# Kernel optimization log

Measured on AMD Instinct MI355X. Metric: run time of the kernel, lower is better.

## Reference

```python
import jax, jax.numpy as jnp
import numpy as np

B, S, D, H = 2, 2048, 1024, 16
DK = D // H


def setup_inputs() -> dict:
    key = jax.random.key(0)
    ks = jax.random.split(key, 11)
    s = 1.0 / np.sqrt(D)
    inp = {
        "q": jax.random.normal(ks[0], (B, S, D), jnp.float32),
        "k": jax.random.normal(ks[1], (B, S, D), jnp.float32),
        "v": jax.random.normal(ks[2], (B, S, D), jnp.float32),
        "mask": jnp.tril(jnp.ones((S, S), jnp.int32))[None, None],  # [1,1,S,S] causal
        "Wq": jax.random.normal(ks[3], (D, D), jnp.float32) * s,
        "bq": jnp.zeros((D,), jnp.float32),
        "Wk": jax.random.normal(ks[4], (D, D), jnp.float32) * s,
        "bk": jnp.zeros((D,), jnp.float32),
        "Wv": jax.random.normal(ks[5], (D, D), jnp.float32) * s,
        "bv": jnp.zeros((D,), jnp.float32),
        "Wo": jax.random.normal(ks[6], (D, D), jnp.float32) * s,
        "bo": jnp.zeros((D,), jnp.float32),
    }
    return inp


def reference(q, k, v, mask, Wq, bq, Wk, bk, Wv, bv, Wo, bo):
    # projections -> [B, H, S, DK]
    def split_heads(x):
        return x.reshape(B, S, H, DK).transpose(0, 2, 1, 3)

    Q = split_heads(q @ Wq + bq)
    K = split_heads(k @ Wk + bk)
    V = split_heads(v @ Wv + bv)

    scores = jnp.einsum("bhqd,bhkd->bhqk", Q, K) / jnp.sqrt(jnp.float32(DK))
    scores = jnp.where(mask == 0, jnp.float32(-1e9), scores)
    # source applies dropout(p=0.0) here -> identity
    attn = jax.nn.softmax(scores, axis=-1)  # [B,H,S,S]
    x = jnp.einsum("bhqk,bhkd->bhqd", attn, V)
    x = x.transpose(0, 2, 1, 3).reshape(B, S, D)
    return x @ Wo + bo
```

## Files before the change

kernel.cpp:

```cpp
#include <hip/hip_runtime.h>
#include <hip/hip_bf16.h>
#include <stdint.h>

#define Bb 2
#define Ss 2048
#define Dd 1024
#define Hh 16
#define DKk 64

#define QSCALE 0.180336878f

typedef __attribute__((ext_vector_type(8))) short s8v;
typedef __attribute__((ext_vector_type(4))) short s4v;
typedef __attribute__((ext_vector_type(4))) float f4v;
typedef __attribute__((ext_vector_type(16))) float f16v;

#if __has_builtin(__builtin_amdgcn_exp2f)
#define EXP2(x) __builtin_amdgcn_exp2f(x)
#else
#define EXP2(x) __expf((x)*0.69314718f)
#endif

__device__ __forceinline__ unsigned short f2bf(float f) {
    __hip_bfloat16 h = __float2bfloat16(f);
    union { __hip_bfloat16 h; unsigned short u; } c; c.h = h;
    return c.u;
}

__device__ __forceinline__ unsigned pack_bf2(float lo, float hi) {
    __hip_bfloat162 h = __float22bfloat162_rn(float2{lo, hi});
    union { __hip_bfloat162 h; unsigned u; } c; c.h = h;
    return c.u;
}

__device__ __forceinline__ void gload16(const void* g, void* l) {
    __builtin_amdgcn_global_load_lds((__attribute__((address_space(1))) void*)g,
                                     (__attribute__((address_space(3))) void*)l, 16, 0, 0);
}

__global__ void __launch_bounds__(256) prep_x(const float* __restrict__ q,
                                              const float* __restrict__ k,
                                              const float* __restrict__ v,
                                              unsigned short* __restrict__ xq,
                                              unsigned short* __restrict__ xk,
                                              unsigned short* __restrict__ xv) {
    const int z = blockIdx.z;
    const float* s = (z == 0) ? q : ((z == 1) ? k : v);
    unsigned short* d = (z == 0) ? xq : ((z == 1) ? xk : xv);
    long i = ((long)blockIdx.x * blockDim.x + threadIdx.x) * 8;
    f4v a = *(const f4v*)(s + i);
    f4v b = *(const f4v*)(s + i + 4);
    union { unsigned u[4]; s8v v; } o;
    o.u[0] = pack_bf2(a[0], a[1]);
    o.u[1] = pack_bf2(a[2], a[3]);
    o.u[2] = pack_bf2(b[0], b[1]);
    o.u[3] = pack_bf2(b[2], b[3]);
    *(s8v*)(void*)(d + i) = o.v;
}

__global__ void __launch_bounds__(256) prep_w(const float* __restrict__ Wq,
                                              const float* __restrict__ Wk,
                                              const float* __restrict__ Wv,
                                              const float* __restrict__ Wo,
                                              unsigned short* __restrict__ o0,
                                              unsigned short* __restrict__ o1,
                                              unsigned short* __restrict__ o2,
                                              unsigned short* __restrict__ o3) {
    __shared__ float t[64][65];
    const int z = blockIdx.z;
    const float* W = (z == 0) ? Wq : ((z == 1) ? Wk : ((z == 2) ? Wv : Wo));
    unsigned short* O = (z == 0) ? o0 : ((z == 1) ? o1 : ((z == 2) ? o2 : o3));
    const int n0 = (blockIdx.x & 15) * 64;
    const int k0 = (blockIdx.x >> 4) * 64;
    const int c = threadIdx.x & 63;
    const int r4 = threadIdx.x >> 6;
#pragma unroll
    for (int i = 0; i < 16; i++) {
        int r = i * 4 + r4;
        t[r][c] = W[(long)(k0 + r) * Dd + n0 + c];
    }
    __syncthreads();
#pragma unroll
    for (int i = 0; i < 16; i++) {
        int r = i * 4 + r4;
        O[(long)(n0 + r) * Dd + k0 + c] = f2bf(t[c][r]);
    }
}

template <int MODE>
__device__ __forceinline__ void gemm_body(const unsigned short* __restrict__ A,
                                          const unsigned short* __restrict__ Bt,
                                          const float* __restrict__ bias,
                                          void* __restrict__ out, float oscale,
                                          unsigned short* smem) {
    unsigned short* As = smem;
    unsigned short* Bs = smem + 128 * 64;
    const int tid = threadIdx.x;
    const int l = tid & 63;
    const int w = tid >> 6;
    const int wr = w >> 1, wc = w & 1;
    const int lr = l & 15, lg = l >> 4;
    const int m0 = blockIdx.y * 128;
    const int n0 = blockIdx.x * 128;

    f4v acc[4][4];
#pragma unroll
    for (int m = 0; m < 4; m++)
#pragma unroll
        for (int n = 0; n < 4; n++) acc[m][n] = (f4v){0.f, 0.f, 0.f, 0.f};

    const int srow = tid >> 3;
    const int sg = (tid & 7) ^ (srow & 7);
    char* lbaseA = (char*)As + w * 1024;
    char* lbaseB = (char*)Bs + w * 1024;

    for (int t = 0; t < 16; t++) {
        const int k0 = t * 64;
#pragma unroll
        for (int i = 0; i < 4; i++) {
            int rowA = i * 32 + srow;
            gload16((const char*)A + ((long)(m0 + rowA) * 1024 + k0) * 2 + sg * 16,
                    lbaseA + i * 4096);
            gload16((const char*)Bt + ((long)(n0 + rowA) * 1024 + k0) * 2 + sg * 16,
                    lbaseB + i * 4096);
        }
        __syncthreads();
#pragma unroll
        for (int kk = 0; kk < 2; kk++) {
            s8v af[4], bfr[4];
#pragma unroll
            for (int m = 0; m < 4; m++) {
                int row = wr * 64 + m * 16 + lr;
                int gc = (kk * 4 + lg) ^ (row & 7);
                af[m] = *(const s8v*)((const char*)As + row * 128 + gc * 16);
            }
#pragma unroll
            for (int n = 0; n < 4; n++) {
                int row = wc * 64 + n * 16 + lr;
                int gc = (kk * 4 + lg) ^ (row & 7);
                bfr[n] = *(const s8v*)((const char*)Bs + row * 128 + gc * 16);
            }
#pragma unroll
            for (int m = 0; m < 4; m++)
#pragma unroll
                for (int n = 0; n < 4; n++)
                    acc[m][n] = __builtin_amdgcn_mfma_f32_16x16x32_bf16(af[m], bfr[n],
                                                                        acc[m][n], 0, 0, 0);
        }
        __syncthreads();
    }

#pragma unroll
    for (int n = 0; n < 4; n++) {
        int col = n0 + wc * 64 + n * 16 + lr;
        float bv = bias[col];
#pragma unroll
        for (int m = 0; m < 4; m++) {
#pragma unroll
            for (int r = 0; r < 4; r++) {
                int row = m0 + wr * 64 + m * 16 + lg * 4 + r;
                float val = acc[m][n][r] + bv;
                if (MODE == 0) {
                    int b = row >> 11, s2 = row & 2047, h = col >> 6, d = col & 63;
                    ((unsigned short*)out)[(((b * Hh + h) * Ss + s2) << 6) + d] =
                        f2bf(val * oscale);
                } else if (MODE == 1) {
                    int b = row >> 11, s2 = row & 2047, h = col >> 6, d = col & 63;
                    ((unsigned short*)out)[((b * Hh + h) * DKk + d) * Ss + s2] = f2bf(val);
                } else {
                    ((float*)out)[(long)row * Dd + col] = val;
                }
            }
        }
    }
}

__global__ void __launch_bounds__(256) qkv_gemm(const unsigned short* __restrict__ xq,
                                                const unsigned short* __restrict__ xk,
                                                const unsigned short* __restrict__ xv,
                                                const unsigned short* __restrict__ Wqt,
                                                const unsigned short* __restrict__ Wkt,
                                                const unsigned short* __restrict__ Wvt,
                                                const float* __restrict__ bq,
                                                const float* __restrict__ bk,
                                                const float* __restrict__ bv,
                                                unsigned short* __restrict__ Qh,
                                                unsigned short* __restrict__ Kh,
                                                unsigned short* __restrict__ Vt) {
    __shared__ unsigned short smem[128 * 64 * 2];
    const int z = blockIdx.z;
    if (z == 0)
        gemm_body<0>(xq, Wqt, bq, Qh, QSCALE, smem);
    else if (z == 1)
        gemm_body<0>(xk, Wkt, bk, Kh, 1.f, smem);
    else
        gemm_body<1>(xv, Wvt, bv, Vt, 1.f, smem);
}

__global__ void __launch_bounds__(256) out_gemm(const unsigned short* __restrict__ x,
                                                const unsigned short* __restrict__ Wot,
                                                const float* __restrict__ bo,
                                                float* __restrict__ out) {
    __shared__ unsigned short smem[128 * 64 * 2];
    gemm_body<2>(x, Wot, bo, out, 1.f, smem);
}

__global__ void __launch_bounds__(256) attn_kernel(const unsigned short* __restrict__ Qh,
                                                   const unsigned short* __restrict__ Kh,
                                                   const unsigned short* __restrict__ Vt,
                                                   unsigned short* __restrict__ xatt) {
    __shared__ __align__(16) char ldsbuf[32768];
    unsigned short* Ks = (unsigned short*)ldsbuf;
    unsigned short* Vs = (unsigned short*)(ldsbuf + 16384);
    const int tid = threadIdx.x;
    const int w = tid >> 6, l = tid & 63;
    const int lq = l & 31;
    const int hi = l >> 5;
    const int bh = blockIdx.x & 31;
    const int tile = 63 - (blockIdx.x >> 5);
    const int q0 = tile * 32;
    const int b = bh >> 4, h = bh & 15;
    const unsigned short* Qp = Qh + bh * Ss * DKk;
    const unsigned short* Kp = Kh + bh * Ss * DKk;
    const unsigned short* Vp = Vt + bh * DKk * Ss;

    s8v qf[4];
#pragma unroll
    for (int kk = 0; kk < 4; kk++)
        qf[kk] = *(const s8v*)(Qp + (q0 + lq) * 64 + kk * 16 + hi * 8);

    f16v oT0, oT1;
#pragma unroll
    for (int r = 0; r < 16; r++) { oT0[r] = 0.f; oT1[r] = 0.f; }
    float mx = -1e30f, sm = 0.f;
    const int nkb = tile + 1;
    const int nch = (nkb + 3) >> 2;

    for (int ch = 0; ch < nch; ch++) {
        const int kv0 = ch * 128;
#pragma unroll
        for (int i = 0; i < 4; i++) {
            const int G0 = i * 256 + w * 64;
            int G = G0 + l;
            int row = G >> 3, gd = G & 7;
            int gs = gd ^ (row & 7);
            gload16(Kp + (kv0 + row) * 64 + gs * 8, (char*)Ks + G0 * 16);
        }
#pragma unroll
        for (int i = 0; i < 4; i++) {
            const int G0 = i * 256 + w * 64;
            int G = G0 + l;
            int row = G >> 4, gd = G & 15;
            int gs = gd ^ (row & 15);
            gload16(Vp + (long)row * Ss + kv0 + gs * 8, (char*)Vs + G0 * 16);
        }
        __syncthreads();

        const int kb = ch * 4 + w;
        if (kb < nkb) {
            const int k0 = kb * 32;
            s8v kf[4];
#pragma unroll
            for (int kk = 0; kk < 4; kk++) {
                int row = w * 32 + lq;
                int g = (2 * kk + hi) ^ (row & 7);
                kf[kk] = *(const s8v*)((const char*)Ks + (row * 8 + g) * 16);
            }
            s8v vf0[2], vf1[2];
#pragma unroll
            for (int kk = 0; kk < 2; kk++) {
                int g0 = 4 * w + 2 * kk + hi;
                vf0[kk] = *(const s8v*)((const char*)Vs + (lq * 16 + (g0 ^ (lq & 15))) * 16);
                vf1[kk] =
                    *(const s8v*)((const char*)Vs + ((32 + lq) * 16 + (g0 ^ (lq & 15))) * 16);
            }

            f16v S;
#pragma unroll
            for (int r = 0; r < 16; r++) S[r] = 0.f;
#pragma unroll
            for (int kk = 0; kk < 4; kk++)
                S = __builtin_amdgcn_mfma_f32_32x32x16_bf16(kf[kk], qf[kk], S, 0, 0, 0);

            const bool diag = (kb == nkb - 1);
            float e[16];
#pragma unroll
            for (int r = 0; r < 16; r++) {
                float v = S[r];
                if (diag) {
                    int kv = k0 + (r & 3) + 8 * (r >> 2) + 4 * hi;
                    if (kv > q0 + lq) v = -1e30f;
                }
                e[r] = v;
            }
            float m8[8];
#pragma unroll
            for (int i = 0; i < 8; i++) m8[i] = fmaxf(e[i], e[i + 8]);
#pragma unroll
            for (int i = 0; i < 4; i++) m8[i] = fmaxf(m8[i], m8[i + 4]);
            float pmax = fmaxf(fmaxf(m8[0], m8[1]), fmaxf(m8[2], m8[3]));
            pmax = fmaxf(pmax, __shfl_xor(pmax, 32));

            if (!__all(pmax - mx <= 8.f)) {
                float mn = fmaxf(mx, pmax);
                float sc = EXP2(mx - mn);
                mx = mn;
                sm *= sc;
#pragma unroll
                for (int r = 0; r < 16; r++) { oT0[r] *= sc; oT1[r] *= sc; }
            }
#pragma unroll
            for (int r = 0; r < 16; r++) e[r] = EXP2(e[r] - mx);
            float s8s[8];
#pragma unroll
            for (int i = 0; i < 8; i++) s8s[i] = e[i] + e[i + 8];
#pragma unroll
            for (int i = 0; i < 4; i++) s8s[i] = s8s[i] + s8s[i + 4];
            float rs = (s8s[0] + s8s[1]) + (s8s[2] + s8s[3]);
            sm += rs + __shfl_xor(rs, 32);

            unsigned pk[8], sw[8];
#pragma unroll
            for (int i = 0; i < 8; i++) pk[i] = pack_bf2(e[2 * i], e[2 * i + 1]);
#pragma unroll
            for (int i = 0; i < 8; i++) sw[i] = (unsigned)__shfl_xor((int)pk[i], 32);
            union { unsigned u[4]; s8v v; } p0, p1;
            p0.u[0] = hi ? sw[2] : pk[0];
            p0.u[1] = hi ? sw[3] : pk[1];
            p0.u[2] = hi ? pk[2] : sw[0];
            p0.u[3] = hi ? pk[3] : sw[1];
            p1.u[0] = hi ? sw[6] : pk[4];
            p1.u[1] = hi ? sw[7] : pk[5];
            p1.u[2] = hi ? pk[6] : sw[4];
            p1.u[3] = hi ? pk[7] : sw[5];

            oT0 = __builtin_amdgcn_mfma_f32_32x32x16_bf16(vf0[0], p0.v, oT0, 0, 0, 0);
            oT0 = __builtin_amdgcn_mfma_f32_32x32x16_bf16(vf0[1], p1.v, oT0, 0, 0, 0);
            oT1 = __builtin_amdgcn_mfma_f32_32x32x16_bf16(vf1[0], p0.v, oT1, 0, 0, 0);
            oT1 = __builtin_amdgcn_mfma_f32_32x32x16_bf16(vf1[1], p1.v, oT1, 0, 0, 0);
        }
        __syncthreads();
    }

    float(*plds)[64][34] = (float(*)[64][34])ldsbuf;
    if (w >= 2) {
        float* p = plds[w - 2][l];
        p[0] = mx; p[1] = sm;
#pragma unroll
        for (int r = 0; r < 16; r++) { p[2 + r] = oT0[r]; p[18 + r] = oT1[r]; }
    }
    __syncthreads();
    if (w < 2) {
        const float* p = plds[w][l];
        float m2 = p[0], s2 = p[1];
        float M = fmaxf(mx, m2);
        float a = EXP2(mx - M), bb = EXP2(m2 - M);
        sm = sm * a + s2 * bb;
#pragma unroll
        for (int r = 0; r < 16; r++) {
            oT0[r] = oT0[r] * a + p[2 + r] * bb;
            oT1[r] = oT1[r] * a + p[18 + r] * bb;
        }
        mx = M;
    }
    __syncthreads();
    if (w == 1) {
        float* p = plds[0][l];
        p[0] = mx; p[1] = sm;
#pragma unroll
        for (int r = 0; r < 16; r++) { p[2 + r] = oT0[r]; p[18 + r] = oT1[r]; }
    }
    __syncthreads();
    if (w != 0) return;
    {
        const float* p = plds[0][l];
        float m2 = p[0], s2 = p[1];
        float M = fmaxf(mx, m2);
        float a = EXP2(mx - M), bb = EXP2(m2 - M);
        sm = sm * a + s2 * bb;
#pragma unroll
        for (int r = 0; r < 16; r++) {
            oT0[r] = oT0[r] * a + p[2 + r] * bb;
            oT1[r] = oT1[r] * a + p[18 + r] * bb;
        }
    }

    const float inv = 1.f / sm;
    const int q = q0 + lq;
    unsigned short* orow = xatt + (long)(b * Ss + q) * Dd + h * 64;
#pragma unroll
    for (int g = 0; g < 4; g++) {
        union { unsigned u[2]; s4v v; } v0, v1;
        v0.u[0] = pack_bf2(oT0[g * 4 + 0] * inv, oT0[g * 4 + 1] * inv);
        v0.u[1] = pack_bf2(oT0[g * 4 + 2] * inv, oT0[g * 4 + 3] * inv);
        v1.u[0] = pack_bf2(oT1[g * 4 + 0] * inv, oT1[g * 4 + 1] * inv);
        v1.u[1] = pack_bf2(oT1[g * 4 + 2] * inv, oT1[g * 4 + 3] * inv);
        int d = 8 * g + 4 * hi;
        *(s4v*)(orow + d) = v0.v;
        *(s4v*)(orow + 32 + d) = v1.v;
    }
}

extern "C" void kernel_launch(void* const* d_in, const int* in_sizes, int n_in,
                              void* d_out, int out_size, void* d_ws, size_t ws_size,
                              hipStream_t stream) {
    const float* q  = (const float*)d_in[0];
    const float* k  = (const float*)d_in[1];
    const float* v  = (const float*)d_in[2];
    const float* Wq = (const float*)d_in[4];
    const float* bq = (const float*)d_in[5];
    const float* Wk = (const float*)d_in[6];
    const float* bk = (const float*)d_in[7];
    const float* Wv = (const float*)d_in[8];
    const float* bv = (const float*)d_in[9];
    const float* Wo = (const float*)d_in[10];
    const float* bo = (const float*)d_in[11];
    float* out = (float*)d_out;

    char* ws = (char*)d_ws;
    unsigned short* xq  = (unsigned short*)(ws + 0);
    unsigned short* xk  = (unsigned short*)(ws + 8388608);
    unsigned short* xv  = (unsigned short*)(ws + 16777216);
    unsigned short* Wqt = (unsigned short*)(ws + 25165824);
    unsigned short* Wkt = (unsigned short*)(ws + 27262976);
    unsigned short* Wvt = (unsigned short*)(ws + 29360128);
    unsigned short* Wot = (unsigned short*)(ws + 31457280);
    unsigned short* Qh  = (unsigned short*)(ws + 33554432);
    unsigned short* Kh  = (unsigned short*)(ws + 41943040);
    unsigned short* Vtp = (unsigned short*)(ws + 50331648);
    unsigned short* xat = (unsigned short*)(ws + 58720256);

    prep_x<<<dim3(2048, 1, 3), 256, 0, stream>>>(q, k, v, xq, xk, xv);
    prep_w<<<dim3(256, 1, 4), 256, 0, stream>>>(Wq, Wk, Wv, Wo, Wqt, Wkt, Wvt, Wot);
    qkv_gemm<<<dim3(8, 32, 3), 256, 0, stream>>>(xq, xk, xv, Wqt, Wkt, Wvt,
                                                 bq, bk, bv, Qh, Kh, Vtp);
    attn_kernel<<<dim3(2048), 256, 0, stream>>>(Qh, Kh, Vtp, xat);
    out_gemm<<<dim3(8, 32), 256, 0, stream>>>(xat, Wot, bo, out);
}
```

Baseline: 149.2 us.

## Double-buffer K/V tiles in attention kernel with async prefetch and MFMA priority

Doubles the attention kernel's LDS buffer to 64KB and prefetches the next 128-key K/V chunk into the alternate buffer while the current chunk is computed. Explicit vmcnt waits and raw s_barrier replace __syncthreads, and s_setprio raises wave priority around the MFMA groups. The aim is to hide global-to-LDS load latency behind compute. In exchange, the larger LDS footprint can reduce occupancy, and the hand-counted vmcnt(8) relies on gload16 issuing exactly one counted load per call.

After: 151.8 us. Within noise of the previous version (+1.7%).

```diff
diff --git a/kernel.cpp b/kernel.cpp
--- a/kernel.cpp
+++ b/kernel.cpp
@@ -209,9 +209,7 @@
                                                    const unsigned short* __restrict__ Kh,
                                                    const unsigned short* __restrict__ Vt,
                                                    unsigned short* __restrict__ xatt) {
-    __shared__ __align__(16) char ldsbuf[32768];
-    unsigned short* Ks = (unsigned short*)ldsbuf;
-    unsigned short* Vs = (unsigned short*)(ldsbuf + 16384);
+    __shared__ __align__(16) char ldsbuf[65536];
     const int tid = threadIdx.x;
     const int w = tid >> 6, l = tid & 63;
     const int lq = l & 31;
@@ -228,6 +226,7 @@
 #pragma unroll
     for (int kk = 0; kk < 4; kk++)
         qf[kk] = *(const s8v*)(Qp + (q0 + lq) * 64 + kk * 16 + hi * 8);
+    asm volatile("" :: "v"(qf[0]), "v"(qf[1]), "v"(qf[2]), "v"(qf[3]));
 
     f16v oT0, oT1;
 #pragma unroll
@@ -236,26 +235,40 @@
     const int nkb = tile + 1;
     const int nch = (nkb + 3) >> 2;
 
+#define STAGE(ch_, p_)                                                          \
+    do {                                                                        \
+        const int kv0_ = (ch_) * 128;                                           \
+        char* Kb_ = ldsbuf + (p_) * 32768;                                      \
+        char* Vb_ = Kb_ + 16384;                                                \
+        _Pragma("unroll") for (int i_ = 0; i_ < 4; i_++) {                      \
+            const int G0_ = i_ * 256 + w * 64;                                  \
+            int G_ = G0_ + l;                                                   \
+            int row_ = G_ >> 3, gd_ = G_ & 7;                                   \
+            int gs_ = gd_ ^ (row_ & 7);                                         \
+            gload16(Kp + (kv0_ + row_) * 64 + gs_ * 8, Kb_ + G0_ * 16);         \
+        }                                                                       \
+        _Pragma("unroll") for (int i_ = 0; i_ < 4; i_++) {                      \
+            const int G0_ = i_ * 256 + w * 64;                                  \
+            int G_ = G0_ + l;                                                   \
+            int row_ = G_ >> 4, gd_ = G_ & 15;                                  \
+            int gs_ = gd_ ^ (row_ & 15);                                        \
+            gload16(Vp + (long)row_ * Ss + kv0_ + gs_ * 8, Vb_ + G0_ * 16);     \
+        }                                                                       \
+    } while (0)
+
+    STAGE(0, 0);
+    int cur = 0;
     for (int ch = 0; ch < nch; ch++) {
-        const int kv0 = ch * 128;
-#pragma unroll
-        for (int i = 0; i < 4; i++) {
-            const int G0 = i * 256 + w * 64;
-            int G = G0 + l;
-            int row = G >> 3, gd = G & 7;
-            int gs = gd ^ (row & 7);
-            gload16(Kp + (kv0 + row) * 64 + gs * 8, (char*)Ks + G0 * 16);
-        }
-#pragma unroll
-        for (int i = 0; i < 4; i++) {
-            const int G0 = i * 256 + w * 64;
-            int G = G0 + l;
-            int row = G >> 4, gd = G & 15;
-            int gs = gd ^ (row & 15);
-            gload16(Vp + (long)row * Ss + kv0 + gs * 8, (char*)Vs + G0 * 16);
-        }
-        __syncthreads();
-
+        if (ch + 1 < nch) {
+            STAGE(ch + 1, cur ^ 1);
+            asm volatile("s_waitcnt vmcnt(8)" ::: "memory");
+        } else {
+            asm volatile("s_waitcnt vmcnt(0)" ::: "memory");
+        }
+        __builtin_amdgcn_s_barrier();
+
+        const char* Kb = ldsbuf + cur * 32768;
+        const char* Vb = Kb + 16384;
         const int kb = ch * 4 + w;
         if (kb < nkb) {
             const int k0 = kb * 32;
@@ -264,23 +277,24 @@
             for (int kk = 0; kk < 4; kk++) {
                 int row = w * 32 + lq;
                 int g = (2 * kk + hi) ^ (row & 7);
-                kf[kk] = *(const s8v*)((const char*)Ks + (row * 8 + g) * 16);
+                kf[kk] = *(const s8v*)(Kb + (row * 8 + g) * 16);
             }
             s8v vf0[2], vf1[2];
 #pragma unroll
             for (int kk = 0; kk < 2; kk++) {
                 int g0 = 4 * w + 2 * kk + hi;
-                vf0[kk] = *(const s8v*)((const char*)Vs + (lq * 16 + (g0 ^ (lq & 15))) * 16);
-                vf1[kk] =
-                    *(const s8v*)((const char*)Vs + ((32 + lq) * 16 + (g0 ^ (lq & 15))) * 16);
+                vf0[kk] = *(const s8v*)(Vb + (lq * 16 + (g0 ^ (lq & 15))) * 16);
+                vf1[kk] = *(const s8v*)(Vb + ((32 + lq) * 16 + (g0 ^ (lq & 15))) * 16);
             }
 
             f16v S;
 #pragma unroll
             for (int r = 0; r < 16; r++) S[r] = 0.f;
+            __builtin_amdgcn_s_setprio(1);
 #pragma unroll
             for (int kk = 0; kk < 4; kk++)
                 S = __builtin_amdgcn_mfma_f32_32x32x16_bf16(kf[kk], qf[kk], S, 0, 0, 0);
+            __builtin_amdgcn_s_setprio(0);
 
             const bool diag = (kb == nkb - 1);
             float e[16];
@@ -334,13 +348,17 @@
             p1.u[2] = hi ? pk[6] : sw[4];
             p1.u[3] = hi ? pk[7] : sw[5];
 
+            __builtin_amdgcn_s_setprio(1);
             oT0 = __builtin_amdgcn_mfma_f32_32x32x16_bf16(vf0[0], p0.v, oT0, 0, 0, 0);
             oT0 = __builtin_amdgcn_mfma_f32_32x32x16_bf16(vf0[1], p1.v, oT0, 0, 0, 0);
             oT1 = __builtin_amdgcn_mfma_f32_32x32x16_bf16(vf1[0], p0.v, oT1, 0, 0, 0);
             oT1 = __builtin_amdgcn_mfma_f32_32x32x16_bf16(vf1[1], p1.v, oT1, 0, 0, 0);
-        }
-        __syncthreads();
-    }
+            __builtin_amdgcn_s_setprio(0);
+        }
+        __builtin_amdgcn_s_barrier();
+        cur ^= 1;
+    }
+#undef STAGE
 
     float(*plds)[64][34] = (float(*)[64][34])ldsbuf;
     if (w >= 2) {
```

## Share K/V LDS tiles across two query tiles per 512-thread attention block

Applied to the files above, without the earlier changes.

The attention kernel now runs 512 threads per block covering two adjacent 32-row query tiles. Both wave groups consume the same K/V chunks staged in LDS, so each chunk is loaded once for 64 queries instead of 32, halving global K/V traffic per query and the grid size. LDS grows to hold two sets of reduction scratch. The cost is that the lower query tile's waves sit idle on the final diagonal block, and larger blocks may lower occupancy or scheduling flexibility.

Result: slower. 152.2 us (+2.0%).

```diff
diff --git a/kernel.cpp b/kernel.cpp
--- a/kernel.cpp
+++ b/kernel.cpp
@@ -205,20 +205,21 @@
     gemm_body<2>(x, Wot, bo, out, 1.f, smem);
 }
 
-__global__ void __launch_bounds__(256) attn_kernel(const unsigned short* __restrict__ Qh,
+__global__ void __launch_bounds__(512) attn_kernel(const unsigned short* __restrict__ Qh,
                                                    const unsigned short* __restrict__ Kh,
                                                    const unsigned short* __restrict__ Vt,
                                                    unsigned short* __restrict__ xatt) {
-    __shared__ __align__(16) char ldsbuf[32768];
+    __shared__ __align__(16) char ldsbuf[34816];
     unsigned short* Ks = (unsigned short*)ldsbuf;
     unsigned short* Vs = (unsigned short*)(ldsbuf + 16384);
     const int tid = threadIdx.x;
     const int w = tid >> 6, l = tid & 63;
+    const int g = w >> 2, wg = w & 3;
     const int lq = l & 31;
     const int hi = l >> 5;
     const int bh = blockIdx.x & 31;
-    const int tile = 63 - (blockIdx.x >> 5);
-    const int q0 = tile * 32;
+    const int tile = 31 - (blockIdx.x >> 5);
+    const int q0 = tile * 64 + g * 32;
     const int b = bh >> 4, h = bh & 15;
     const unsigned short* Qp = Qh + bh * Ss * DKk;
     const unsigned short* Kp = Kh + bh * Ss * DKk;
@@ -228,27 +229,28 @@
 #pragma unroll
     for (int kk = 0; kk < 4; kk++)
         qf[kk] = *(const s8v*)(Qp + (q0 + lq) * 64 + kk * 16 + hi * 8);
+    asm volatile("" :: "v"(qf[0]), "v"(qf[1]), "v"(qf[2]), "v"(qf[3]));
 
     f16v oT0, oT1;
 #pragma unroll
     for (int r = 0; r < 16; r++) { oT0[r] = 0.f; oT1[r] = 0.f; }
     float mx = -1e30f, sm = 0.f;
-    const int nkb = tile + 1;
-    const int nch = (nkb + 3) >> 2;
+    const int nkb = 2 * tile + 1 + g;
+    const int nch = (2 * tile + 2 + 3) >> 2;
 
     for (int ch = 0; ch < nch; ch++) {
         const int kv0 = ch * 128;
 #pragma unroll
-        for (int i = 0; i < 4; i++) {
-            const int G0 = i * 256 + w * 64;
+        for (int i = 0; i < 2; i++) {
+            const int G0 = i * 512 + w * 64;
             int G = G0 + l;
             int row = G >> 3, gd = G & 7;
             int gs = gd ^ (row & 7);
             gload16(Kp + (kv0 + row) * 64 + gs * 8, (char*)Ks + G0 * 16);
         }
 #pragma unroll
-        for (int i = 0; i < 4; i++) {
-            const int G0 = i * 256 + w * 64;
+        for (int i = 0; i < 2; i++) {
+            const int G0 = i * 512 + w * 64;
             int G = G0 + l;
             int row = G >> 4, gd = G & 15;
             int gs = gd ^ (row & 15);
@@ -256,20 +258,20 @@
         }
         __syncthreads();
 
-        const int kb = ch * 4 + w;
+        const int kb = ch * 4 + wg;
         if (kb < nkb) {
             const int k0 = kb * 32;
             s8v kf[4];
 #pragma unroll
             for (int kk = 0; kk < 4; kk++) {
-                int row = w * 32 + lq;
-                int g = (2 * kk + hi) ^ (row & 7);
-                kf[kk] = *(const s8v*)((const char*)Ks + (row * 8 + g) * 16);
+                int row = wg * 32 + lq;
+                int gidx = (2 * kk + hi) ^ (row & 7);
+                kf[kk] = *(const s8v*)((const char*)Ks + (row * 8 + gidx) * 16);
             }
             s8v vf0[2], vf1[2];
 #pragma unroll
             for (int kk = 0; kk < 2; kk++) {
-                int g0 = 4 * w + 2 * kk + hi;
+                int g0 = 4 * wg + 2 * kk + hi;
                 vf0[kk] = *(const s8v*)((const char*)Vs + (lq * 16 + (g0 ^ (lq & 15))) * 16);
                 vf1[kk] =
                     *(const s8v*)((const char*)Vs + ((32 + lq) * 16 + (g0 ^ (lq & 15))) * 16);
@@ -342,16 +344,16 @@
         __syncthreads();
     }
 
-    float(*plds)[64][34] = (float(*)[64][34])ldsbuf;
-    if (w >= 2) {
-        float* p = plds[w - 2][l];
+    float(*plds)[2][64][34] = (float(*)[2][64][34])ldsbuf;
+    if (wg >= 2) {
+        float* p = plds[g][wg - 2][l];
         p[0] = mx; p[1] = sm;
 #pragma unroll
         for (int r = 0; r < 16; r++) { p[2 + r] = oT0[r]; p[18 + r] = oT1[r]; }
     }
     __syncthreads();
-    if (w < 2) {
-        const float* p = plds[w][l];
+    if (wg < 2) {
+        const float* p = plds[g][wg][l];
         float m2 = p[0], s2 = p[1];
         float M = fmaxf(mx, m2);
         float a = EXP2(mx - M), bb = EXP2(m2 - M);
@@ -364,16 +366,16 @@
         mx = M;
     }
     __syncthreads();
-    if (w == 1) {
-        float* p = plds[0][l];
+    if (wg == 1) {
+        float* p = plds[g][0][l];
         p[0] = mx; p[1] = sm;
 #pragma unroll
         for (int r = 0; r < 16; r++) { p[2 + r] = oT0[r]; p[18 + r] = oT1[r]; }
     }
     __syncthreads();
-    if (w != 0) return;
+    if (wg != 0) return;
     {
-        const float* p = plds[0][l];
+        const float* p = plds[g][0][l];
         float m2 = p[0], s2 = p[1];
         float M = fmaxf(mx, m2);
         float a = EXP2(mx - M), bb = EXP2(m2 - M);
@@ -389,13 +391,13 @@
     const int q = q0 + lq;
     unsigned short* orow = xatt + (long)(b * Ss + q) * Dd + h * 64;
 #pragma unroll
-    for (int g = 0; g < 4; g++) {
+    for (int gg = 0; gg < 4; gg++) {
         union { unsigned u[2]; s4v v; } v0, v1;
-        v0.u[0] = pack_bf2(oT0[g * 4 + 0] * inv, oT0[g * 4 + 1] * inv);
-        v0.u[1] = pack_bf2(oT0[g * 4 + 2] * inv, oT0[g * 4 + 3] * inv);
-        v1.u[0] = pack_bf2(oT1[g * 4 + 0] * inv, oT1[g * 4 + 1] * inv);
-        v1.u[1] = pack_bf2(oT1[g * 4 + 2] * inv, oT1[g * 4 + 3] * inv);
-        int d = 8 * g + 4 * hi;
+        v0.u[0] = pack_bf2(oT0[gg * 4 + 0] * inv, oT0[gg * 4 + 1] * inv);
+        v0.u[1] = pack_bf2(oT0[gg * 4 + 2] * inv, oT0[gg * 4 + 3] * inv);
+        v1.u[0] = pack_bf2(oT1[gg * 4 + 0] * inv, oT1[gg * 4 + 1] * inv);
+        v1.u[1] = pack_bf2(oT1[gg * 4 + 2] * inv, oT1[gg * 4 + 3] * inv);
+        int d = 8 * gg + 4 * hi;
         *(s4v*)(orow + d) = v0.v;
         *(s4v*)(orow + 32 + d) = v1.v;
     }
@@ -434,6 +436,6 @@
     prep_w<<<dim3(256, 1, 4), 256, 0, stream>>>(Wq, Wk, Wv, Wo, Wqt, Wkt, Wvt, Wot);
     qkv_gemm<<<dim3(8, 32, 3), 256, 0, stream>>>(xq, xk, xv, Wqt, Wkt, Wvt,
                                                  bq, bk, bv, Qh, Kh, Vtp);
-    attn_kernel<<<dim3(2048), 256, 0, stream>>>(Qh, Kh, Vtp, xat);
+    attn_kernel<<<dim3(1024), 512, 0, stream>>>(Qh, Kh, Vtp, xat);
     out_gemm<<<dim3(8, 32), 256, 0, stream>>>(xat, Wot, bo, out);
 }
```
